# Optimization experiments

Measured on AMD Instinct MI355X. Metric: run time of the kernel, lower is better.

## Reference

```python
import jax, jax.numpy as jnp
import numpy as np
import math

B, C, W = 4, 256, 64
GROUPS = 32
EPS = 1e-6


def setup_inputs() -> dict:
    key = jax.random.key(0)
    ks = jax.random.split(key, 6)
    xavier = math.sqrt(2.0 / (C + C))
    return {
        "x": jax.random.normal(ks[0], (B, C, W, W), dtype=jnp.float32),
        "gn_gamma": jnp.ones((C,), dtype=jnp.float32),
        "gn_beta": jnp.zeros((C,), dtype=jnp.float32),
        "wq": jax.random.normal(ks[1], (C, C), dtype=jnp.float32) * xavier,
        "bq": jnp.zeros((C,), dtype=jnp.float32),
        "wk": jax.random.normal(ks[2], (C, C), dtype=jnp.float32) * xavier,
        "bk": jnp.zeros((C,), dtype=jnp.float32),
        "wv": jax.random.normal(ks[3], (C, C), dtype=jnp.float32) * xavier,
        "bv": jnp.zeros((C,), dtype=jnp.float32),
        "wo": jax.random.normal(ks[4], (C, C), dtype=jnp.float32) * 1e-5,
        "bo": jnp.zeros((C,), dtype=jnp.float32),
    }


def _nin(w, b, t):
    # 1x1 conv via shared weights: [O,C] x [B,C,H,W] -> [B,O,H,W]
    return jnp.einsum('oc,bchw->bohw', w, t) + b[None, :, None, None]


def _group_norm(x, gamma, beta):
    b, c, h, w = x.shape
    xr = x.reshape(b, GROUPS, c // GROUPS, h, w)
    mu = xr.mean(axis=(2, 3, 4), keepdims=True)
    var = xr.var(axis=(2, 3, 4), keepdims=True)
    xn = ((xr - mu) / jnp.sqrt(var + EPS)).reshape(b, c, h, w)
    return xn * gamma[None, :, None, None] + beta[None, :, None, None]


def reference(x, gn_gamma, gn_beta, wq, bq, wk, bk, wv, bv, wo, bo):
    b, c, wdt, _ = x.shape
    n = wdt * wdt  # number of spatial tokens
    h = _group_norm(x, gn_gamma, gn_beta)
    q = _nin(wq, bq, h).reshape(b, c, n)
    k = _nin(wk, bk, h).reshape(b, c, n)
    v = _nin(wv, bv, h).reshape(b, c, n)
    scale = 1.0 / math.sqrt(c)
    scores = jnp.einsum('bcn,bcm->bnm', q, k) * scale  # [B, N, N]
    attn = jax.nn.softmax(scores, axis=-1)
    o = jnp.einsum('bnm,bcm->bcn', attn, v).reshape(b, c, wdt, wdt)
    return x + _nin(wo, bo, o)
```

## Files before the change

### kernel.cpp

```cpp
#include <hip/hip_runtime.h>
#include <math.h>

#define B_      4
#define C_      256
#define NTOK    4096
#define GROUPS_ 32
#define CPG_    8
#define EPS_    1e-6f
#define QSCALE  0.0625f
#define NSEG    4
#define KSEG    (NTOK / NSEG)
#define QB      128

typedef __attribute__((ext_vector_type(8)))  short short8v;
typedef __attribute__((ext_vector_type(4)))  float float4v;
typedef __attribute__((ext_vector_type(16))) float f32x16;
typedef __attribute__((ext_vector_type(4)))  unsigned short ushort4v;
typedef unsigned short ushort_t;

__device__ __forceinline__ ushort_t f2bf(float f) {
  union { float f; unsigned u; } v; v.f = f;
  unsigned r = (v.u + 0x7FFFu + ((v.u >> 16) & 1u)) >> 16;
  return (ushort_t)r;
}
__device__ __forceinline__ float bf2f(ushort_t u) {
  union { unsigned u; float f; } v; v.u = ((unsigned)u) << 16; return v.f;
}

__device__ __forceinline__ float4v mfma16(short8v a, short8v b, float4v c) {
  return __builtin_amdgcn_mfma_f32_16x16x32_bf16(a, b, c, 0, 0, 0);
}
__device__ __forceinline__ f32x16 mfma32(short8v a, short8v b, f32x16 c) {
  return __builtin_amdgcn_mfma_f32_32x32x16_bf16(a, b, c, 0, 0, 0);
}

__device__ __forceinline__ void gld16(const ushort_t* g, ushort_t* l) {
  __builtin_amdgcn_global_load_lds(
      (const __attribute__((address_space(1))) unsigned int*)g,
      (__attribute__((address_space(3))) unsigned int*)l, 16, 0, 0);
}

__global__ __launch_bounds__(256) void gn_stats(const float* __restrict__ x,
                                                float* __restrict__ stats) {
  const int bg = blockIdx.x;
  const size_t base = (size_t)bg * CPG_ * NTOK;
  const int t = threadIdx.x;
  float s = 0.f, s2 = 0.f;
  for (int i = t * 4; i < CPG_ * NTOK; i += 1024) {
    float4 v = *reinterpret_cast<const float4*>(x + base + i);
    s  += v.x + v.y + v.z + v.w;
    s2 += v.x * v.x + v.y * v.y + v.z * v.z + v.w * v.w;
  }
  #pragma unroll
  for (int m = 32; m >= 1; m >>= 1) { s += __shfl_xor(s, m); s2 += __shfl_xor(s2, m); }
  __shared__ float red[8];
  const int wv = t >> 6;
  if ((t & 63) == 0) { red[wv] = s; red[4 + wv] = s2; }
  __syncthreads();
  if (t == 0) {
    float ts  = red[0] + red[1] + red[2] + red[3];
    float ts2 = red[4] + red[5] + red[6] + red[7];
    const float inv_n = 1.0f / (float)(CPG_ * NTOK);
    float mu  = ts * inv_n;
    float var = ts2 * inv_n - mu * mu;
    stats[bg * 2]     = mu;
    stats[bg * 2 + 1] = rsqrtf(var + EPS_);
  }
}

__global__ __launch_bounds__(256) void gn_apply(
    const float* __restrict__ x, const float* __restrict__ gamma,
    const float* __restrict__ beta, const float* __restrict__ stats,
    ushort_t* __restrict__ Ht) {
  const int b  = blockIdx.y;
  const int n0 = blockIdx.x * 64;
  const int t  = threadIdx.x;
  __shared__ __align__(16) ushort_t Hs[64][264];
  const float* xb = x + (size_t)b * C_ * NTOK;
  #pragma unroll
  for (int it = 0; it < 16; ++it) {
    const int idx = t + 256 * it;
    const int c   = idx >> 4;
    const int ch  = (idx & 15) * 4;
    float4 v = *reinterpret_cast<const float4*>(xb + (size_t)c * NTOK + n0 + ch);
    const float mu = stats[(b * GROUPS_ + (c >> 3)) * 2];
    const float rs = stats[(b * GROUPS_ + (c >> 3)) * 2 + 1];
    const float ga = gamma[c] * rs;
    const float be = beta[c] - mu * ga;
    Hs[ch + 0][c] = f2bf(v.x * ga + be);
    Hs[ch + 1][c] = f2bf(v.y * ga + be);
    Hs[ch + 2][c] = f2bf(v.z * ga + be);
    Hs[ch + 3][c] = f2bf(v.w * ga + be);
  }
  __syncthreads();
  ushort_t* Hb = Ht + (size_t)b * NTOK * C_;
  #pragma unroll
  for (int it = 0; it < 8; ++it) {
    const int idx = t + 256 * it;
    const int row = idx >> 5;
    const int ch  = (idx & 31) * 8;
    *reinterpret_cast<short8v*>(Hb + (size_t)(n0 + row) * C_ + ch) =
        *reinterpret_cast<const short8v*>(&Hs[row][ch]);
  }
}

__global__ __launch_bounds__(256) void wconv(
    const float* __restrict__ wq, const float* __restrict__ wk,
    const float* __restrict__ wv, const float* __restrict__ wo,
    ushort_t* __restrict__ Wb) {
  const int m = blockIdx.y;
  const float* srcs[4] = {wq, wk, wv, wo};
  const float* s = srcs[m];
  const int i = (blockIdx.x * 256 + threadIdx.x) * 4;
  float4 v = *reinterpret_cast<const float4*>(s + i);
  ushort4v o4 = {f2bf(v.x), f2bf(v.y), f2bf(v.z), f2bf(v.w)};
  *reinterpret_cast<ushort4v*>(Wb + (size_t)m * 65536 + i) = o4;
}

template <int MODE>
__global__ __launch_bounds__(256) void nin_mfma(
    const ushort_t* __restrict__ Wb, const float* __restrict__ bias,
    const ushort_t* __restrict__ Hin, const float* __restrict__ xres,
    void* __restrict__ outp, float oscale) {
  const int b  = blockIdx.y;
  const int n0 = blockIdx.x * 32;
  const int t  = threadIdx.x;
  const int w  = t >> 6, l = t & 63;
  const int lg = l >> 4, ln = l & 15;
  __shared__ __align__(16) ushort_t Hs[32][264];
  const ushort_t* Hb = Hin + (size_t)b * NTOK * C_;
  #pragma unroll
  for (int it = 0; it < 4; ++it) {
    const int idx = t + 256 * it;
    const int row = idx >> 5;
    const int ch  = (idx & 31) * 8;
    *reinterpret_cast<short8v*>(&Hs[row][ch]) =
        *reinterpret_cast<const short8v*>(Hb + (size_t)(n0 + row) * C_ + ch);
  }
  __syncthreads();

  float4v acc[4][2];
  #pragma unroll
  for (int mt = 0; mt < 4; ++mt)
    #pragma unroll
    for (int nt = 0; nt < 2; ++nt) acc[mt][nt] = (float4v){0.f, 0.f, 0.f, 0.f};

  const ushort_t* Wrow = Wb + (size_t)(64 * w + ln) * C_;
  #pragma unroll
  for (int kk = 0; kk < 8; ++kk) {
    short8v af[4], bfr[2];
    #pragma unroll
    for (int mt = 0; mt < 4; ++mt)
      af[mt] = *reinterpret_cast<const short8v*>(Wrow + mt * 16 * C_ + kk * 32 + 8 * lg);
    #pragma unroll
    for (int nt = 0; nt < 2; ++nt)
      bfr[nt] = *reinterpret_cast<const short8v*>(&Hs[nt * 16 + ln][kk * 32 + 8 * lg]);
    #pragma unroll
    for (int mt = 0; mt < 4; ++mt)
      #pragma unroll
      for (int nt = 0; nt < 2; ++nt)
        acc[mt][nt] = mfma16(af[mt], bfr[nt], acc[mt][nt]);
  }

  #pragma unroll
  for (int mt = 0; mt < 4; ++mt) {
    const int mb = 64 * w + mt * 16 + 4 * lg;
    #pragma unroll
    for (int nt = 0; nt < 2; ++nt) {
      const int n = n0 + nt * 16 + ln;
      if (MODE == 0) {
        ushort4v pk;
        #pragma unroll
        for (int r = 0; r < 4; ++r)
          pk[r] = f2bf((acc[mt][nt][r] + bias[mb + r]) * oscale);
        *reinterpret_cast<ushort4v*>((ushort_t*)outp + ((size_t)b * NTOK + n) * C_ + mb) = pk;
      } else if (MODE == 1) {
        const int k  = n & 31, kb = n >> 5;
        const int e  = (k & 3) | (((k >> 3) & 1) << 2);
        const int o  = ((k >> 2) & 1) | (((k >> 4) & 1) << 1);
        #pragma unroll
        for (int r = 0; r < 4; ++r) {
          const int c = mb + r;
          const int s = o ^ ((c >> 1) & 3);
          ((ushort_t*)outp)[((size_t)b * (NTOK / 32) + kb) * (C_ * 32)
                            + (size_t)c * 32 + s * 8 + e] =
              f2bf(acc[mt][nt][r] + bias[mb + r]);
        }
      } else {
        #pragma unroll
        for (int r = 0; r < 4; ++r) {
          const size_t off = ((size_t)b * C_ + mb + r) * NTOK + n;
          ((float*)outp)[off] = acc[mt][nt][r] + bias[mb + r] + xres[off];
        }
      }
    }
  }
}

__global__ __launch_bounds__(256, 2) void flash6(
    const ushort_t* __restrict__ Qt, const ushort_t* __restrict__ Kt,
    const ushort_t* __restrict__ Vg, ushort_t* __restrict__ O0,
    ushort_t* __restrict__ Orest, float2* __restrict__ ml) {
  const int id  = blockIdx.x;
  const int xcd = id & 7, sq = id >> 3;
  const int combo = xcd + 8 * (sq >> 5);
  const int b   = combo & 3;
  const int seg = combo >> 2;
  const int q0  = (sq & 31) * QB;
  const int t = threadIdx.x, w = t >> 6, l = t & 63;
  const int ln = l & 31, hi = l >> 5;

  __shared__ __align__(16) ushort_t Ks[2][32][256];
  __shared__ __align__(16) ushort_t Vs[2][8192];

  const ushort_t* Kb_ = Kt + (size_t)b * NTOK * C_;
  const ushort_t* Vb_ = Vg + (size_t)b * NTOK * C_;

  short8v qf[16];
  {
    const ushort_t* qrow = Qt + ((size_t)b * NTOK + q0 + 32 * w + ln) * C_ + 8 * hi;
    #pragma unroll
    for (int kk = 0; kk < 16; ++kk)
      qf[kk] = *reinterpret_cast<const short8v*>(qrow + 16 * kk);
  }

  f32x16 Oacc[8];
  #pragma unroll
  for (int ct = 0; ct < 8; ++ct)
    #pragma unroll
    for (int r = 0; r < 16; ++r) Oacc[ct][r] = 0.f;
  float m_run = -1e30f, l_run = 0.f;

  const int kbase = seg * KSEG;
  const int NT = KSEG / 32;

  auto STAGE_K = [&](int buf, int k0) {
    #pragma unroll
    for (int j = 0; j < 4; ++j) {
      const int i   = 4 * w + j;
      const int row = 2 * i + (l >> 5);
      const int nn  = (l & 31) ^ (row & 15);
      gld16(Kb_ + (size_t)(k0 + row) * C_ + 8 * nn, &Ks[buf][2 * i][0]);
    }
  };
  auto STAGE_V = [&](int buf, int k0) {
    const ushort_t* vt = Vb_ + (size_t)(k0 >> 5) * (C_ * 32);
    #pragma unroll
    for (int j = 0; j < 4; ++j) {
      const int i = 4 * w + j;
      gld16(vt + i * 512 + 8 * l, &Vs[buf][i * 512]);
    }
  };

  int cur = 0;
  STAGE_K(0, kbase);
  STAGE_V(0, kbase);

  for (int it = 0; it < NT; ++it) {
    asm volatile("s_waitcnt vmcnt(4)" ::: "memory");
    __builtin_amdgcn_sched_barrier(0);
    __syncthreads();
    const bool pre = (it + 1 < NT);
    if (pre) {
      const int nxt = kbase + 32 * (it + 1);
      STAGE_K(cur ^ 1, nxt);
      STAGE_V(cur ^ 1, nxt);
    }

    f32x16 sA, sB;
    #pragma unroll
    for (int r = 0; r < 16; ++r) { sA[r] = 0.f; sB[r] = 0.f; }
    const ushort_t* Kc = &Ks[cur][0][0];
    __builtin_amdgcn_s_setprio(1);
    #pragma unroll
    for (int kk = 0; kk < 16; kk += 2) {
      short8v k0f = *reinterpret_cast<const short8v*>(
          Kc + ln * 256 + 8 * ((2 * kk + hi) ^ (ln & 15)));
      short8v k1f = *reinterpret_cast<const short8v*>(
          Kc + ln * 256 + 8 * ((2 * kk + 2 + hi) ^ (ln & 15)));
      sA = mfma32(k0f, qf[kk], sA);
      sB = mfma32(k1f, qf[kk + 1], sB);
    }
    __builtin_amdgcn_s_setprio(0);
    f32x16 sacc = sA + sB;

    float mx8[8];
    #pragma unroll
    for (int j = 0; j < 8; ++j) mx8[j] = fmaxf(sacc[j], sacc[j + 8]);
    #pragma unroll
    for (int j = 0; j < 4; ++j) mx8[j] = fmaxf(mx8[j], mx8[j + 4]);
    float pmax = fmaxf(fmaxf(mx8[0], mx8[2]), fmaxf(mx8[1], mx8[3]));
    pmax = fmaxf(pmax, __shfl_xor(pmax, 32));
    if (!__all(pmax - m_run <= 8.0f)) {
      const float mnew = fmaxf(m_run, pmax);
      const float alpha = __expf(m_run - mnew);
      m_run = mnew;
      l_run *= alpha;
      float av[16];
      #pragma unroll
      for (int r = 0; r < 16; ++r)
        av[r] = __shfl(alpha, (r & 3) + 8 * (r >> 2) + 4 * hi);
      #pragma unroll
      for (int ct = 0; ct < 8; ++ct)
        #pragma unroll
        for (int r = 0; r < 16; ++r) Oacc[ct][r] *= av[r];
    }
    float sm8[8];
    #pragma unroll
    for (int r = 0; r < 16; ++r) sacc[r] = __expf(sacc[r] - m_run);
    #pragma unroll
    for (int j = 0; j < 8; ++j) sm8[j] = sacc[j] + sacc[j + 8];
    #pragma unroll
    for (int j = 0; j < 4; ++j) sm8[j] += sm8[j + 4];
    float ps = (sm8[0] + sm8[2]) + (sm8[1] + sm8[3]);
    ps += __shfl_xor(ps, 32);
    l_run += ps;

    short8v pa0, pa1;
    #pragma unroll
    for (int j = 0; j < 8; ++j) {
      pa0[j] = (short)f2bf(sacc[j]);
      pa1[j] = (short)f2bf(sacc[8 + j]);
    }

    if (pre) asm volatile("s_waitcnt vmcnt(8)" ::: "memory");
    else     asm volatile("s_waitcnt vmcnt(0)" ::: "memory");
    __builtin_amdgcn_sched_barrier(0);
    __syncthreads();

    const ushort_t* Vc = &Vs[cur][0];
    const int sx = (ln >> 1) & 3;
    __builtin_amdgcn_s_setprio(1);
    #pragma unroll
    for (int ct = 0; ct < 8; ++ct) {
      const int c = 32 * ct + ln;
      const ushort_t* vr = Vc + c * 32;
      short8v v0 = *reinterpret_cast<const short8v*>(vr + 8 * (hi ^ sx));
      short8v v1 = *reinterpret_cast<const short8v*>(vr + 8 * ((2 | hi) ^ sx));
      Oacc[ct] = mfma32(pa0, v0, Oacc[ct]);
      Oacc[ct] = mfma32(pa1, v1, Oacc[ct]);
    }
    __builtin_amdgcn_s_setprio(0);
    cur ^= 1;
  }

  ushort_t* Op = (seg == 0 ? O0 : Orest + (size_t)(seg - 1) * (size_t)B_ * NTOK * C_)
               + (size_t)b * NTOK * C_;
  #pragma unroll
  for (int ct = 0; ct < 8; ++ct)
    #pragma unroll
    for (int r = 0; r < 16; ++r) {
      const int qr = q0 + 32 * w + (r & 3) + 8 * (r >> 2) + 4 * hi;
      Op[(size_t)qr * C_ + 32 * ct + ln] = f2bf(Oacc[ct][r]);
    }
  if (hi == 0)
    ml[(seg * B_ + b) * NTOK + q0 + 32 * w + ln] = make_float2(m_run, l_run);
}

__global__ __launch_bounds__(256) void combine_k(
    const ushort_t* __restrict__ O0, const ushort_t* __restrict__ Orest,
    const float2* __restrict__ ml, ushort_t* __restrict__ Ot) {
  const int idx = blockIdx.x * 256 + threadIdx.x;
  const int c8 = idx & 31;
  const int bq = idx >> 5;
  const int b = bq >> 12, q = bq & (NTOK - 1);
  float m4[NSEG], l4[NSEG];
  float M = -1e30f;
  #pragma unroll
  for (int s = 0; s < NSEG; ++s) {
    float2 v = ml[(s * B_ + b) * NTOK + q];
    m4[s] = v.x; l4[s] = v.y;
    M = fmaxf(M, v.x);
  }
  float L = 0.f, wsc[NSEG];
  #pragma unroll
  for (int s = 0; s < NSEG; ++s) { wsc[s] = __expf(m4[s] - M); L += wsc[s] * l4[s]; }
  const float inv = 1.0f / L;
  float acc[8];
  #pragma unroll
  for (int j = 0; j < 8; ++j) acc[j] = 0.f;
  const size_t SLOT = (size_t)B_ * NTOK * C_;
  #pragma unroll
  for (int s = 0; s < NSEG; ++s) {
    const ushort_t* op = (s == 0 ? O0 : Orest + (size_t)(s - 1) * SLOT);
    short8v v = *reinterpret_cast<const short8v*>(op + (size_t)bq * C_ + 8 * c8);
    #pragma unroll
    for (int j = 0; j < 8; ++j) acc[j] += wsc[s] * bf2f((ushort_t)v[j]);
  }
  short8v o8;
  #pragma unroll
  for (int j = 0; j < 8; ++j) o8[j] = (short)f2bf(acc[j] * inv);
  *reinterpret_cast<short8v*>(Ot + (size_t)bq * C_ + 8 * c8) = o8;
}

extern "C" void kernel_launch(void* const* d_in, const int* in_sizes, int n_in,
                              void* d_out, int out_size, void* d_ws, size_t ws_size,
                              hipStream_t stream) {
  (void)in_sizes; (void)n_in; (void)out_size; (void)ws_size;
  const float* x     = (const float*)d_in[0];
  const float* gamma = (const float*)d_in[1];
  const float* beta  = (const float*)d_in[2];
  const float* wq    = (const float*)d_in[3];
  const float* bq    = (const float*)d_in[4];
  const float* wk    = (const float*)d_in[5];
  const float* bk    = (const float*)d_in[6];
  const float* wv    = (const float*)d_in[7];
  const float* bv    = (const float*)d_in[8];
  const float* wo    = (const float*)d_in[9];
  const float* bo    = (const float*)d_in[10];
  float* out = (float*)d_out;

  ushort_t* ws16 = (ushort_t*)d_ws;
  const size_t SLOT = (size_t)B_ * NTOK * C_;

  ushort_t* Ht  = ws16;
  ushort_t* Qt  = ws16 + SLOT;
  ushort_t* Kt  = ws16 + 2 * SLOT;
  ushort_t* Vb  = ws16 + 3 * SLOT;
  ushort_t* OpR = ws16 + 4 * SLOT;
  ushort_t* Op0 = Ht;
  ushort_t* Ot  = Qt;
  ushort_t* Wb  = ws16 + 7 * SLOT;
  float*  stats = (float*)(Wb + 4 * 65536);
  float2* mlp   = (float2*)(stats + 256);

  gn_stats<<<dim3(B_ * GROUPS_), 256, 0, stream>>>(x, stats);
  gn_apply<<<dim3(NTOK / 64, B_), 256, 0, stream>>>(x, gamma, beta, stats, Ht);
  wconv<<<dim3(64, 4), 256, 0, stream>>>(wq, wk, wv, wo, Wb);

  dim3 gg(NTOK / 32, B_);
  nin_mfma<0><<<gg, 256, 0, stream>>>(Wb,             bq, Ht, nullptr, Qt, QSCALE);
  nin_mfma<0><<<gg, 256, 0, stream>>>(Wb + 65536,     bk, Ht, nullptr, Kt, 1.0f);
  nin_mfma<1><<<gg, 256, 0, stream>>>(Wb + 2 * 65536, bv, Ht, nullptr, Vb, 1.0f);

  flash6<<<dim3(NSEG * B_ * (NTOK / QB)), 256, 0, stream>>>(Qt, Kt, Vb, Op0, OpR, mlp);
  combine_k<<<dim3(B_ * NTOK * C_ / 8 / 256), 256, 0, stream>>>(Op0, OpR, mlp, Ot);

  nin_mfma<2><<<gg, 256, 0, stream>>>(Wb + 3 * 65536, bo, Ot, x, out, 1.0f);
}
```

Measured before the change: 170.5 us.

## Fuse QKV projections, software-pipeline PV in flash, fuse combine into output projection

Merges the three Q/K/V 1x1-conv launches into one kernel that reuses the staged H tile, and folds the split-softmax combine into the output projection kernel, so two launches and an intermediate bf16 O round-trip go away. The flash kernel now defers each PV MFMA block to the next iteration using a triple-buffered V tile. That drops the second barrier per iteration and overlaps PV with the next QK^T/softmax. It also uses packed bf16 conversion instructions. The cost is more LDS per block and a more complex buffer-reuse protocol that could raise occupancy pressure or race if the waits are wrong.

```diff
diff --git a/kernel.cpp b/kernel.cpp
--- a/kernel.cpp
+++ b/kernel.cpp
@@ -25,6 +25,11 @@
 }
 __device__ __forceinline__ float bf2f(ushort_t u) {
   union { unsigned u; float f; } v; v.u = ((unsigned)u) << 16; return v.f;
+}
+__device__ __forceinline__ unsigned cvtpk(float lo, float hi) {
+  unsigned r;
+  asm("v_cvt_pk_bf16_f32 %0, %1, %2" : "=v"(r) : "v"(lo), "v"(hi));
+  return r;
 }
 
 __device__ __forceinline__ float4v mfma16(short8v a, short8v b, float4v c) {
@@ -117,11 +122,12 @@
   *reinterpret_cast<ushort4v*>(Wb + (size_t)m * 65536 + i) = o4;
 }
 
-template <int MODE>
-__global__ __launch_bounds__(256) void nin_mfma(
-    const ushort_t* __restrict__ Wb, const float* __restrict__ bias,
-    const ushort_t* __restrict__ Hin, const float* __restrict__ xres,
-    void* __restrict__ outp, float oscale) {
+__global__ __launch_bounds__(256) void nin_qkv(
+    const ushort_t* __restrict__ Wb, const float* __restrict__ bq,
+    const float* __restrict__ bk, const float* __restrict__ bv,
+    const ushort_t* __restrict__ Hin,
+    ushort_t* __restrict__ Qt, ushort_t* __restrict__ Kt,
+    ushort_t* __restrict__ Vv) {
   const int b  = blockIdx.y;
   const int n0 = blockIdx.x * 32;
   const int t  = threadIdx.x;
@@ -139,65 +145,72 @@
   }
   __syncthreads();
 
+  auto gemm = [&](const ushort_t* W, float4v acc[4][2]) {
+    #pragma unroll
+    for (int mt = 0; mt < 4; ++mt)
+      #pragma unroll
+      for (int nt = 0; nt < 2; ++nt) acc[mt][nt] = (float4v){0.f, 0.f, 0.f, 0.f};
+    const ushort_t* Wrow = W + (size_t)(64 * w + ln) * C_;
+    #pragma unroll
+    for (int kk = 0; kk < 8; ++kk) {
+      short8v af[4], bfr[2];
+      #pragma unroll
+      for (int mt = 0; mt < 4; ++mt)
+        af[mt] = *reinterpret_cast<const short8v*>(Wrow + mt * 16 * C_ + kk * 32 + 8 * lg);
+      #pragma unroll
+      for (int nt = 0; nt < 2; ++nt)
+        bfr[nt] = *reinterpret_cast<const short8v*>(&Hs[nt * 16 + ln][kk * 32 + 8 * lg]);
+      #pragma unroll
+      for (int mt = 0; mt < 4; ++mt)
+        #pragma unroll
+        for (int nt = 0; nt < 2; ++nt)
+          acc[mt][nt] = mfma16(af[mt], bfr[nt], acc[mt][nt]);
+    }
+  };
+
   float4v acc[4][2];
   #pragma unroll
-  for (int mt = 0; mt < 4; ++mt)
-    #pragma unroll
-    for (int nt = 0; nt < 2; ++nt) acc[mt][nt] = (float4v){0.f, 0.f, 0.f, 0.f};
-
-  const ushort_t* Wrow = Wb + (size_t)(64 * w + ln) * C_;
-  #pragma unroll
-  for (int kk = 0; kk < 8; ++kk) {
-    short8v af[4], bfr[2];
-    #pragma unroll
-    for (int mt = 0; mt < 4; ++mt)
-      af[mt] = *reinterpret_cast<const short8v*>(Wrow + mt * 16 * C_ + kk * 32 + 8 * lg);
-    #pragma unroll
-    for (int nt = 0; nt < 2; ++nt)
-      bfr[nt] = *reinterpret_cast<const short8v*>(&Hs[nt * 16 + ln][kk * 32 + 8 * lg]);
-    #pragma unroll
-    for (int mt = 0; mt < 4; ++mt)
-      #pragma unroll
-      for (int nt = 0; nt < 2; ++nt)
-        acc[mt][nt] = mfma16(af[mt], bfr[nt], acc[mt][nt]);
-  }
-
-  #pragma unroll
-  for (int mt = 0; mt < 4; ++mt) {
-    const int mb = 64 * w + mt * 16 + 4 * lg;
-    #pragma unroll
-    for (int nt = 0; nt < 2; ++nt) {
-      const int n = n0 + nt * 16 + ln;
-      if (MODE == 0) {
+  for (int m = 0; m < 2; ++m) {
+    const float* bias = (m == 0) ? bq : bk;
+    const float osc = (m == 0) ? QSCALE : 1.0f;
+    ushort_t* dst = (m == 0) ? Qt : Kt;
+    gemm(Wb + (size_t)m * 65536, acc);
+    #pragma unroll
+    for (int mt = 0; mt < 4; ++mt) {
+      const int mb = 64 * w + mt * 16 + 4 * lg;
+      #pragma unroll
+      for (int nt = 0; nt < 2; ++nt) {
+        const int n = n0 + nt * 16 + ln;
         ushort4v pk;
         #pragma unroll
         for (int r = 0; r < 4; ++r)
-          pk[r] = f2bf((acc[mt][nt][r] + bias[mb + r]) * oscale);
-        *reinterpret_cast<ushort4v*>((ushort_t*)outp + ((size_t)b * NTOK + n) * C_ + mb) = pk;
-      } else if (MODE == 1) {
-        const int k  = n & 31, kb = n >> 5;
-        const int e  = (k & 3) | (((k >> 3) & 1) << 2);
-        const int o  = ((k >> 2) & 1) | (((k >> 4) & 1) << 1);
-        #pragma unroll
-        for (int r = 0; r < 4; ++r) {
-          const int c = mb + r;
-          const int s = o ^ ((c >> 1) & 3);
-          ((ushort_t*)outp)[((size_t)b * (NTOK / 32) + kb) * (C_ * 32)
-                            + (size_t)c * 32 + s * 8 + e] =
-              f2bf(acc[mt][nt][r] + bias[mb + r]);
-        }
-      } else {
-        #pragma unroll
-        for (int r = 0; r < 4; ++r) {
-          const size_t off = ((size_t)b * C_ + mb + r) * NTOK + n;
-          ((float*)outp)[off] = acc[mt][nt][r] + bias[mb + r] + xres[off];
-        }
+          pk[r] = f2bf((acc[mt][nt][r] + bias[mb + r]) * osc);
+        *reinterpret_cast<ushort4v*>(dst + ((size_t)b * NTOK + n) * C_ + mb) = pk;
       }
     }
   }
-}
-
-__global__ __launch_bounds__(256, 2) void flash6(
+  gemm(Wb + 2 * 65536, acc);
+  #pragma unroll
+  for (int mt = 0; mt < 4; ++mt) {
+    const int mb = 64 * w + mt * 16 + 4 * lg;
+    #pragma unroll
+    for (int nt = 0; nt < 2; ++nt) {
+      const int n = n0 + nt * 16 + ln;
+      const int k  = n & 31, kb = n >> 5;
+      const int e  = (k & 3) | (((k >> 3) & 1) << 2);
+      const int o  = ((k >> 2) & 1) | (((k >> 4) & 1) << 1);
+      #pragma unroll
+      for (int r = 0; r < 4; ++r) {
+        const int c = mb + r;
+        const int s = o ^ ((c >> 1) & 3);
+        Vv[((size_t)b * (NTOK / 32) + kb) * (C_ * 32) + (size_t)c * 32 + s * 8 + e] =
+            f2bf(acc[mt][nt][r] + bv[mb + r]);
+      }
+    }
+  }
+}
+
+__global__ __launch_bounds__(256, 2) void flash8(
     const ushort_t* __restrict__ Qt, const ushort_t* __restrict__ Kt,
     const ushort_t* __restrict__ Vg, ushort_t* __restrict__ O0,
     ushort_t* __restrict__ Orest, float2* __restrict__ ml) {
@@ -211,7 +224,7 @@
   const int ln = l & 31, hi = l >> 5;
 
   __shared__ __align__(16) ushort_t Ks[2][32][256];
-  __shared__ __align__(16) ushort_t Vs[2][8192];
+  __shared__ __align__(16) ushort_t Vs[3][8192];
 
   const ushort_t* Kb_ = Kt + (size_t)b * NTOK * C_;
   const ushort_t* Vb_ = Vg + (size_t)b * NTOK * C_;
@@ -230,6 +243,8 @@
     #pragma unroll
     for (int r = 0; r < 16; ++r) Oacc[ct][r] = 0.f;
   float m_run = -1e30f, l_run = 0.f;
+  short8v pa0 = {}, pa1 = {};
+  const int sx = (ln >> 1) & 3;
 
   const int kbase = seg * KSEG;
   const int NT = KSEG / 32;
@@ -251,8 +266,21 @@
       gld16(vt + i * 512 + 8 * l, &Vs[buf][i * 512]);
     }
   };
-
-  int cur = 0;
+  auto PV = [&](int vb) {
+    const ushort_t* Vc = &Vs[vb][0];
+    __builtin_amdgcn_s_setprio(1);
+    #pragma unroll
+    for (int ct = 0; ct < 8; ++ct) {
+      const int c = 32 * ct + ln;
+      const ushort_t* vr = Vc + c * 32;
+      short8v v0 = *reinterpret_cast<const short8v*>(vr + 8 * (hi ^ sx));
+      short8v v1 = *reinterpret_cast<const short8v*>(vr + 8 * ((2 | hi) ^ sx));
+      Oacc[ct] = mfma32(pa0, v0, Oacc[ct]);
+      Oacc[ct] = mfma32(pa1, v1, Oacc[ct]);
+    }
+    __builtin_amdgcn_s_setprio(0);
+  };
+
   STAGE_K(0, kbase);
   STAGE_V(0, kbase);
 
@@ -260,17 +288,16 @@
     asm volatile("s_waitcnt vmcnt(4)" ::: "memory");
     __builtin_amdgcn_sched_barrier(0);
     __syncthreads();
-    const bool pre = (it + 1 < NT);
-    if (pre) {
+    if (it + 1 < NT) {
       const int nxt = kbase + 32 * (it + 1);
-      STAGE_K(cur ^ 1, nxt);
-      STAGE_V(cur ^ 1, nxt);
+      STAGE_K((it + 1) & 1, nxt);
+      STAGE_V((it + 1) % 3, nxt);
     }
 
     f32x16 sA, sB;
     #pragma unroll
     for (int r = 0; r < 16; ++r) { sA[r] = 0.f; sB[r] = 0.f; }
-    const ushort_t* Kc = &Ks[cur][0][0];
+    const ushort_t* Kc = &Ks[it & 1][0][0];
     __builtin_amdgcn_s_setprio(1);
     #pragma unroll
     for (int kk = 0; kk < 16; kk += 2) {
@@ -291,7 +318,11 @@
     for (int j = 0; j < 4; ++j) mx8[j] = fmaxf(mx8[j], mx8[j + 4]);
     float pmax = fmaxf(fmaxf(mx8[0], mx8[2]), fmaxf(mx8[1], mx8[3]));
     pmax = fmaxf(pmax, __shfl_xor(pmax, 32));
-    if (!__all(pmax - m_run <= 8.0f)) {
+    const bool need = !__all(pmax - m_run <= 8.0f);
+
+    if (it > 0) PV((it + 2) % 3);
+
+    if (need) {
       const float mnew = fmaxf(m_run, pmax);
       const float alpha = __expf(m_run - mnew);
       m_run = mnew;
@@ -305,9 +336,10 @@
         #pragma unroll
         for (int r = 0; r < 16; ++r) Oacc[ct][r] *= av[r];
     }
+
+    #pragma unroll
+    for (int r = 0; r < 16; ++r) sacc[r] = __expf(sacc[r] - m_run);
     float sm8[8];
-    #pragma unroll
-    for (int r = 0; r < 16; ++r) sacc[r] = __expf(sacc[r] - m_run);
     #pragma unroll
     for (int j = 0; j < 8; ++j) sm8[j] = sacc[j] + sacc[j + 8];
     #pragma unroll
@@ -315,34 +347,20 @@
     float ps = (sm8[0] + sm8[2]) + (sm8[1] + sm8[3]);
     ps += __shfl_xor(ps, 32);
     l_run += ps;
-
-    short8v pa0, pa1;
-    #pragma unroll
-    for (int j = 0; j < 8; ++j) {
-      pa0[j] = (short)f2bf(sacc[j]);
-      pa1[j] = (short)f2bf(sacc[8 + j]);
-    }
-
-    if (pre) asm volatile("s_waitcnt vmcnt(8)" ::: "memory");
-    else     asm volatile("s_waitcnt vmcnt(0)" ::: "memory");
-    __builtin_amdgcn_sched_barrier(0);
-    __syncthreads();
-
-    const ushort_t* Vc = &Vs[cur][0];
-    const int sx = (ln >> 1) & 3;
-    __builtin_amdgcn_s_setprio(1);
-    #pragma unroll
-    for (int ct = 0; ct < 8; ++ct) {
-      const int c = 32 * ct + ln;
-      const ushort_t* vr = Vc + c * 32;
-      short8v v0 = *reinterpret_cast<const short8v*>(vr + 8 * (hi ^ sx));
-      short8v v1 = *reinterpret_cast<const short8v*>(vr + 8 * ((2 | hi) ^ sx));
-      Oacc[ct] = mfma32(pa0, v0, Oacc[ct]);
-      Oacc[ct] = mfma32(pa1, v1, Oacc[ct]);
-    }
-    __builtin_amdgcn_s_setprio(0);
-    cur ^= 1;
-  }
+    union { unsigned u[4]; short8v v; } P0, P1;
+    #pragma unroll
+    for (int j = 0; j < 4; ++j) {
+      P0.u[j] = cvtpk(sacc[2 * j], sacc[2 * j + 1]);
+      P1.u[j] = cvtpk(sacc[8 + 2 * j], sacc[9 + 2 * j]);
+    }
+    pa0 = P0.v;
+    pa1 = P1.v;
+  }
+
+  asm volatile("s_waitcnt vmcnt(0)" ::: "memory");
+  __builtin_amdgcn_sched_barrier(0);
+  __syncthreads();
+  PV((NT - 1) % 3);
 
   ushort_t* Op = (seg == 0 ? O0 : Orest + (size_t)(seg - 1) * (size_t)B_ * NTOK * C_)
                + (size_t)b * NTOK * C_;
@@ -357,40 +375,87 @@
     ml[(seg * B_ + b) * NTOK + q0 + 32 * w + ln] = make_float2(m_run, l_run);
 }
 
-__global__ __launch_bounds__(256) void combine_k(
+__global__ __launch_bounds__(256) void nin_final(
+    const ushort_t* __restrict__ Wo, const float* __restrict__ bo,
     const ushort_t* __restrict__ O0, const ushort_t* __restrict__ Orest,
-    const float2* __restrict__ ml, ushort_t* __restrict__ Ot) {
-  const int idx = blockIdx.x * 256 + threadIdx.x;
-  const int c8 = idx & 31;
-  const int bq = idx >> 5;
-  const int b = bq >> 12, q = bq & (NTOK - 1);
-  float m4[NSEG], l4[NSEG];
-  float M = -1e30f;
-  #pragma unroll
-  for (int s = 0; s < NSEG; ++s) {
-    float2 v = ml[(s * B_ + b) * NTOK + q];
-    m4[s] = v.x; l4[s] = v.y;
-    M = fmaxf(M, v.x);
-  }
-  float L = 0.f, wsc[NSEG];
-  #pragma unroll
-  for (int s = 0; s < NSEG; ++s) { wsc[s] = __expf(m4[s] - M); L += wsc[s] * l4[s]; }
-  const float inv = 1.0f / L;
-  float acc[8];
-  #pragma unroll
-  for (int j = 0; j < 8; ++j) acc[j] = 0.f;
+    const float2* __restrict__ ml, const float* __restrict__ xres,
+    float* __restrict__ out) {
+  const int b  = blockIdx.y;
+  const int n0 = blockIdx.x * 32;
+  const int t  = threadIdx.x;
+  const int w  = t >> 6, l = t & 63;
+  const int lg = l >> 4, ln = l & 15;
+  __shared__ __align__(16) ushort_t Hs[32][264];
   const size_t SLOT = (size_t)B_ * NTOK * C_;
   #pragma unroll
-  for (int s = 0; s < NSEG; ++s) {
-    const ushort_t* op = (s == 0 ? O0 : Orest + (size_t)(s - 1) * SLOT);
-    short8v v = *reinterpret_cast<const short8v*>(op + (size_t)bq * C_ + 8 * c8);
-    #pragma unroll
-    for (int j = 0; j < 8; ++j) acc[j] += wsc[s] * bf2f((ushort_t)v[j]);
-  }
-  short8v o8;
-  #pragma unroll
-  for (int j = 0; j < 8; ++j) o8[j] = (short)f2bf(acc[j] * inv);
-  *reinterpret_cast<short8v*>(Ot + (size_t)bq * C_ + 8 * c8) = o8;
+  for (int it = 0; it < 4; ++it) {
+    const int idx = t + 256 * it;
+    const int row = idx >> 5;
+    const int ch  = (idx & 31) * 8;
+    const int n   = n0 + row;
+    float m4[NSEG], l4[NSEG], M = -1e30f;
+    #pragma unroll
+    for (int s = 0; s < NSEG; ++s) {
+      float2 v = ml[(s * B_ + b) * NTOK + n];
+      m4[s] = v.x; l4[s] = v.y;
+      M = fmaxf(M, v.x);
+    }
+    float L = 0.f, wsc[NSEG];
+    #pragma unroll
+    for (int s = 0; s < NSEG; ++s) { wsc[s] = __expf(m4[s] - M); L += wsc[s] * l4[s]; }
+    const float inv = 1.0f / L;
+    float acc8[8];
+    #pragma unroll
+    for (int j = 0; j < 8; ++j) acc8[j] = 0.f;
+    #pragma unroll
+    for (int s = 0; s < NSEG; ++s) {
+      const ushort_t* op = (s == 0 ? O0 : Orest + (size_t)(s - 1) * SLOT);
+      short8v v = *reinterpret_cast<const short8v*>(
+          op + ((size_t)b * NTOK + n) * C_ + ch);
+      #pragma unroll
+      for (int j = 0; j < 8; ++j) acc8[j] += wsc[s] * bf2f((ushort_t)v[j]);
+    }
+    union { ushort_t us[8]; short8v v; } o8;
+    #pragma unroll
+    for (int j = 0; j < 8; ++j) o8.us[j] = f2bf(acc8[j] * inv);
+    *reinterpret_cast<short8v*>(&Hs[row][ch]) = o8.v;
+  }
+  __syncthreads();
+
+  float4v acc[4][2];
+  #pragma unroll
+  for (int mt = 0; mt < 4; ++mt)
+    #pragma unroll
+    for (int nt = 0; nt < 2; ++nt) acc[mt][nt] = (float4v){0.f, 0.f, 0.f, 0.f};
+  const ushort_t* Wrow = Wo + (size_t)(64 * w + ln) * C_;
+  #pragma unroll
+  for (int kk = 0; kk < 8; ++kk) {
+    short8v af[4], bfr[2];
+    #pragma unroll
+    for (int mt = 0; mt < 4; ++mt)
+      af[mt] = *reinterpret_cast<const short8v*>(Wrow + mt * 16 * C_ + kk * 32 + 8 * lg);
+    #pragma unroll
+    for (int nt = 0; nt < 2; ++nt)
+      bfr[nt] = *reinterpret_cast<const short8v*>(&Hs[nt * 16 + ln][kk * 32 + 8 * lg]);
+    #pragma unroll
+    for (int mt = 0; mt < 4; ++mt)
+      #pragma unroll
+      for (int nt = 0; nt < 2; ++nt)
+        acc[mt][nt] = mfma16(af[mt], bfr[nt], acc[mt][nt]);
+  }
+  #pragma unroll
+  for (int mt = 0; mt < 4; ++mt) {
+    const int mb = 64 * w + mt * 16 + 4 * lg;
+    #pragma unroll
+    for (int nt = 0; nt < 2; ++nt) {
+      const int n = n0 + nt * 16 + ln;
+      #pragma unroll
+      for (int r = 0; r < 4; ++r) {
+        const size_t off = ((size_t)b * C_ + mb + r) * NTOK + n;
+        out[off] = acc[mt][nt][r] + bo[mb + r] + xres[off];
+      }
+    }
+  }
 }
 
 extern "C" void kernel_launch(void* const* d_in, const int* in_sizes, int n_in,
@@ -419,7 +484,6 @@
   ushort_t* Vb  = ws16 + 3 * SLOT;
   ushort_t* OpR = ws16 + 4 * SLOT;
   ushort_t* Op0 = Ht;
-  ushort_t* Ot  = Qt;
   ushort_t* Wb  = ws16 + 7 * SLOT;
   float*  stats = (float*)(Wb + 4 * 65536);
   float2* mlp   = (float2*)(stats + 256);
@@ -429,12 +493,9 @@
   wconv<<<dim3(64, 4), 256, 0, stream>>>(wq, wk, wv, wo, Wb);
 
   dim3 gg(NTOK / 32, B_);
-  nin_mfma<0><<<gg, 256, 0, stream>>>(Wb,             bq, Ht, nullptr, Qt, QSCALE);
-  nin_mfma<0><<<gg, 256, 0, stream>>>(Wb + 65536,     bk, Ht, nullptr, Kt, 1.0f);
-  nin_mfma<1><<<gg, 256, 0, stream>>>(Wb + 2 * 65536, bv, Ht, nullptr, Vb, 1.0f);
-
-  flash6<<<dim3(NSEG * B_ * (NTOK / QB)), 256, 0, stream>>>(Qt, Kt, Vb, Op0, OpR, mlp);
-  combine_k<<<dim3(B_ * NTOK * C_ / 8 / 256), 256, 0, stream>>>(Op0, OpR, mlp, Ot);
-
-  nin_mfma<2><<<gg, 256, 0, stream>>>(Wb + 3 * 65536, bo, Ot, x, out, 1.0f);
-}
+  nin_qkv<<<gg, 256, 0, stream>>>(Wb, bq, bk, bv, Ht, Qt, Kt, Vb);
+
+  flash8<<<dim3(NSEG * B_ * (NTOK / QB)), 256, 0, stream>>>(Qt, Kt, Vb, Op0, OpR, mlp);
+
+  nin_final<<<gg, 256, 0, stream>>>(Wb + 3 * 65536, bo, Op0, OpR, mlp, x, out);
+}
```

Result: slower. 186.3 us (+9.3%).
